# Performance work log

Hardware: AMD Instinct MI355X
Metric: run time of the kernel (lower is better)

## Reference

```python
import jax, jax.numpy as jnp
from jax import lax
import numpy as np

D_MODEL = 1024
D_STATE = 16
D_CONV = 4
EXPAND = 2
D_INNER = EXPAND * D_MODEL  # 2048
DT_RANK = D_MODEL // 16     # 64
BATCH = 4
SEQ = 1024


def setup_inputs() -> dict:
    key = jax.random.key(0)
    ks = iter(jax.random.split(key, 40))
    def w(shape, s=0.02):
        return (s * jax.random.normal(next(ks), shape)).astype(jnp.float32)
    inp = {"x": jax.random.normal(next(ks), (BATCH, SEQ, D_MODEL), dtype=jnp.float32)}
    # S4D-real style A init: A = -exp(A_log), A_log = log(1..N) per channel
    Alog = jnp.log(jnp.tile(jnp.arange(1, D_STATE + 1, dtype=jnp.float32), (D_INNER, 1)))
    for s in ("f", "b"):
        inp[f"inproj_{s}"] = w((D_MODEL, 2 * D_INNER))
        inp[f"conv_w_{s}"] = w((D_INNER, D_CONV), 0.2)
        inp[f"conv_b_{s}"] = jnp.zeros((D_INNER,), jnp.float32)
        inp[f"xproj_{s}"] = w((D_INNER, DT_RANK + 2 * D_STATE))
        inp[f"dt_w_{s}"] = w((DT_RANK, D_INNER))
        inp[f"dt_b_{s}"] = jnp.full((D_INNER,), -4.0, jnp.float32)  # softplus(-4)~0.018
        inp[f"Alog_{s}"] = Alog
        inp[f"Dp_{s}"] = jnp.ones((D_INNER,), jnp.float32)
        inp[f"outproj_{s}"] = w((D_INNER, D_MODEL))
    inp["gate_w"] = w((2 * D_MODEL, D_MODEL))
    inp["gate_b"] = jnp.zeros((D_MODEL,), jnp.float32)
    inp["proj_w"] = w((D_MODEL, D_MODEL))
    inp["proj_b"] = jnp.zeros((D_MODEL,), jnp.float32)
    return inp


def _mamba(x, inproj, conv_w, conv_b, xproj, dt_w, dt_b, Alog, Dp, outproj):
    B, L, _ = x.shape
    xz = x @ inproj                           # [B,L,2*Di]
    u, z = jnp.split(xz, 2, axis=-1)          # each [B,L,Di]
    # depthwise causal conv1d, width D_CONV
    K = conv_w.shape[1]
    up = jnp.pad(u, ((0, 0), (K - 1, 0), (0, 0)))
    uc = conv_b
    for k in range(K):
        uc = uc + up[:, k:k + L, :] * conv_w[:, k]
    uc = jax.nn.silu(uc)                      # [B,L,Di]
    dbl = uc @ xproj                          # [B,L,dt_rank+2N]
    N = Alog.shape[1]
    dt, Bm, Cm = jnp.split(dbl, [DT_RANK, DT_RANK + N], axis=-1)
    delta = jax.nn.softplus(dt @ dt_w + dt_b) # [B,L,Di]
    A = -jnp.exp(Alog)                        # [Di,N]

    def step(h, inp):
        u_t, d_t, B_t, C_t = inp              # [B,Di],[B,Di],[B,N],[B,N]
        dA = jnp.exp(d_t[..., None] * A)      # [B,Di,N]
        h = dA * h + (d_t * u_t)[..., None] * B_t[:, None, :]
        y_t = jnp.einsum('bdn,bn->bd', h, C_t)
        return h, y_t

    h0 = jnp.zeros((B, uc.shape[-1], N), x.dtype)
    xs = (uc.transpose(1, 0, 2), delta.transpose(1, 0, 2),
          Bm.transpose(1, 0, 2), Cm.transpose(1, 0, 2))
    _, ys = lax.scan(step, h0, xs)            # ys: [L,B,Di]
    y = ys.transpose(1, 0, 2) + uc * Dp
    y = y * jax.nn.silu(z)
    return y @ outproj                        # [B,L,d_model]


def reference(x, inproj_f, conv_w_f, conv_b_f, xproj_f, dt_w_f, dt_b_f, Alog_f, Dp_f, outproj_f,
              inproj_b, conv_w_b, conv_b_b, xproj_b, dt_w_b, dt_b_b, Alog_b, Dp_b, outproj_b,
              gate_w, gate_b, proj_w, proj_b):
    y_f = _mamba(x, inproj_f, conv_w_f, conv_b_f, xproj_f, dt_w_f, dt_b_f, Alog_f, Dp_f, outproj_f)
    xb = jnp.flip(x, axis=1)
    y_b = _mamba(xb, inproj_b, conv_w_b, conv_b_b, xproj_b, dt_w_b, dt_b_b, Alog_b, Dp_b, outproj_b)
    y_b = jnp.flip(y_b, axis=1)
    g = jax.nn.sigmoid(jnp.concatenate([y_f, y_b], axis=-1) @ gate_w + gate_b)
    y = g * y_f + (1.0 - g) * y_b
    return y @ proj_w + proj_b
```

## Files before the change

kernel.cpp:

```cpp
#include <hip/hip_runtime.h>
#include <hip/hip_bf16.h>

#define B_  4
#define L_  1024
#define DM  1024
#define DI  2048
#define NS  16
#define RK  64
#define MT  (B_ * L_)
#define NC  32
#define CH  (L_ / NC)
#define KSX 256
#define NZX 8
#define PSZ (B_ * NC * NS * DI)

typedef unsigned short u16;
typedef __attribute__((ext_vector_type(8))) short  bh8;
typedef __attribute__((ext_vector_type(8))) unsigned short us8;
typedef __attribute__((ext_vector_type(8))) _Float16 h8;
typedef __attribute__((ext_vector_type(4))) float  f4;

__device__ __forceinline__ float bf2f(u16 u) {
  union { unsigned int i; float f; } c; c.i = ((unsigned int)u) << 16; return c.f;
}
__device__ __forceinline__ u16 f2bf(float f) {
  union { float f; unsigned int i; } c; c.f = f;
  unsigned int x = c.i;
  unsigned int r = (x + 0x7fffu + ((x >> 16) & 1u)) >> 16;
  return (u16)r;
}

__device__ __forceinline__ void gl16(const u16* g, u16* l) {
  __builtin_amdgcn_global_load_lds(
      (const __attribute__((address_space(1))) void*)g,
      (__attribute__((address_space(3))) void*)l, 16, 0, 0);
}

__global__ void detect_k(const unsigned int* __restrict__ alog,
                         int* __restrict__ flag, int* __restrict__ afl) {
  *flag = (alog[0] != 0u) ? 1 : 0;
  afl[0] = 1; afl[1] = 1;
}

__global__ __launch_bounds__(256)
void cvt_k(const void* __restrict__ src, u16* __restrict__ dst, int n,
           const int* __restrict__ flag) {
  int i = blockIdx.x * 256 + threadIdx.x;
  if (i >= n) return;
  if (*flag) dst[i] = ((const u16*)src)[i];
  else       dst[i] = f2bf(((const float*)src)[i]);
}

__global__ __launch_bounds__(256)
void cvt10_k(const int* __restrict__ flagp,
             const void* s0, u16* d0, int n0, const void* s1, u16* d1, int n1,
             const void* s2, u16* d2, int n2, const void* s3, u16* d3, int n3,
             const void* s4, u16* d4, int n4, const void* s5, u16* d5, int n5,
             const void* s6, u16* d6, int n6, const void* s7, u16* d7, int n7,
             const void* s8, u16* d8, int n8, const void* s9, u16* d9, int n9)
{
  const void* s; u16* d; int n;
  switch (blockIdx.y) {
    case 0: s = s0; d = d0; n = n0; break;  case 1: s = s1; d = d1; n = n1; break;
    case 2: s = s2; d = d2; n = n2; break;  case 3: s = s3; d = d3; n = n3; break;
    case 4: s = s4; d = d4; n = n4; break;  case 5: s = s5; d = d5; n = n5; break;
    case 6: s = s6; d = d6; n = n6; break;  case 7: s = s7; d = d7; n = n7; break;
    case 8: s = s8; d = d8; n = n8; break;  default: s = s9; d = d9; n = n9; break;
  }
  int i = blockIdx.x * 256 + threadIdx.x;
  if (i >= n) return;
  d[i] = *flagp ? ((const u16*)s)[i] : f2bf(((const float*)s)[i]);
}

__global__ __launch_bounds__(256)
void a2_k(const int* __restrict__ flagp, const void* __restrict__ sf,
          const void* __restrict__ sb, _Float16* __restrict__ A2h,
          int* __restrict__ afl)
{
  int i = blockIdx.x * 256 + threadIdx.x;
  int dir = i >> 15;
  const void* src = dir ? sb : sf;
  int j = i & (DI * NS - 1);
  float v = *flagp ? bf2f(((const u16*)src)[j]) : ((const float*)src)[j];
  float a2 = -__expf(v);
  A2h[i] = (_Float16)a2;
  int n = i & 15;
  if (fabsf(a2 + (float)(n + 1)) > 1e-3f * (n + 1)) atomicAnd(&afl[dir], 0);
}

struct TpBatch {
  const void* src[8];
  u16* dst[8];
  int R[8], C[8], tilesX[8];
  int tOff[9];
  int cnt;
};

__global__ __launch_bounds__(256)
void tposeB_k(TpBatch tb, const int* __restrict__ flag) {
  __shared__ u16 tile[32][33];
  int bid = blockIdx.x;
  int i = 0;
  #pragma unroll
  for (int q = 0; q < 7; ++q) if (i + 1 < tb.cnt && bid >= tb.tOff[i + 1]) ++i;
  int local = bid - tb.tOff[i];
  int tX = tb.tilesX[i];
  int c0 = (local % tX) * 32, r0 = (local / tX) * 32;
  int R = tb.R[i], C = tb.C[i];
  const void* src = tb.src[i];
  u16* dst = tb.dst[i];
  int tx = threadIdx.x & 31, ty = threadIdx.x >> 5;
  int isbf = *flag;
  #pragma unroll
  for (int k = 0; k < 4; ++k) {
    int r = r0 + ty + k * 8, c = c0 + tx;
    u16 v = 0;
    if (r < R && c < C)
      v = isbf ? ((const u16*)src)[(size_t)r * C + c]
               : f2bf(((const float*)src)[(size_t)r * C + c]);
    tile[ty + k * 8][tx] = v;
  }
  __syncthreads();
  #pragma unroll
  for (int k = 0; k < 4; ++k) {
    int c = c0 + ty + k * 8, r = r0 + tx;
    if (c < C && r < R)
      dst[(size_t)c * R + r] = tile[tx][ty + k * 8];
  }
}

template<int ACT, int CATM, int OUTF, int BIDIR, int SPLITK, int DUO, int XSW, int ZDIR>
__global__ __launch_bounds__(256)
void gemm2(const u16* __restrict__ A, int lda,
           const u16* __restrict__ Wt,
           const u16* __restrict__ bias,
           void* __restrict__ Cp, int ldc, void* __restrict__ C2,
           int M, int N, int K,
           const u16* __restrict__ yfp, const u16* __restrict__ ybp,
           const int* __restrict__ flagp, const u16* __restrict__ Aalt)
{
  __shared__ __align__(16) u16 As[128][64];
  __shared__ __align__(16) u16 Bs[128][64];

  int bx, by;
  if (XSW) {
    int g = blockIdx.y * gridDim.x + blockIdx.x;
    int xcd = g & 7, j = g >> 3;
    int bxb = gridDim.x >> 3;
    int sh = 31 - __builtin_clz(bxb);
    bx = xcd * bxb + (j & (bxb - 1));
    by = j >> sh;
  } else { bx = blockIdx.x; by = blockIdx.y; }

  int zdir = 0, zslice = 0;
  if (ZDIR && SPLITK) { zdir = blockIdx.z >> 3; zslice = blockIdx.z & (NZX - 1); }
  else if (ZDIR)      { zdir = blockIdx.z; }
  else if (SPLITK)    { zslice = blockIdx.z; }

  const int tid  = threadIdx.x;
  const int lane = tid & 63;
  const int w    = tid >> 6;
  const int wm   = (w >> 1) * 64, wn = (w & 1) * 64;
  const int bm0  = by * 128, bn0 = bx * 128;
  const int l15  = lane & 15, quad = lane >> 4;
  const int rI8  = lane >> 3;
  const int cG8  = (lane & 7) ^ rI8;

  const u16* Wtp = ZDIR ? (Wt + (size_t)zdir * N * K) : Wt;

  f4 acc[4][4] = {};

  const int kb = SPLITK ? zslice * KSX : 0;
  const int ke = SPLITK ? kb + KSX : K;

  for (int k0 = kb; k0 < ke; k0 += 64) {
    {
      const u16* Abase;
      if (ZDIR)     Abase = zdir ? Aalt : A;
      else if (DUO) Abase = (bn0 < DM) ? A : ybp;
      else          Abase = A;
      #pragma unroll
      for (int t = 0; t < 4; ++t) {
        int rb = w * 32 + t * 8;
        int row = rb + rI8;
        const u16* gp;
        if (CATM) {
          int kk = k0 + cG8 * 8;
          int m = bm0 + row;
          gp = (kk < DM) ? (yfp + (size_t)m * DM + kk)
                         : (ybp + (size_t)(m ^ (L_ - 1)) * DM + (kk - DM));
        } else {
          gp = Abase + (size_t)(bm0 + row) * lda + k0 + cG8 * 8;
        }
        gl16(gp, &As[rb][0]);
      }
    }
    #pragma unroll
    for (int t = 0; t < 4; ++t) {
      int rb = w * 32 + t * 8;
      int row = rb + rI8;
      int n = bn0 + row; if (n > N - 1) n = N - 1;
      gl16(Wtp + (size_t)n * K + k0 + cG8 * 8, &Bs[rb][0]);
    }
    __syncthreads();
    #pragma unroll
    for (int s = 0; s < 2; ++s) {
      bh8 af[4], bg[4];
      const int phys = ((quad + 4 * s) ^ (l15 & 7)) * 8;
      #pragma unroll
      for (int i = 0; i < 4; ++i) {
        af[i] = *(const bh8*)&As[wm + i * 16 + l15][phys];
        bg[i] = *(const bh8*)&Bs[wn + i * 16 + l15][phys];
      }
      #pragma unroll
      for (int i = 0; i < 4; ++i)
        #pragma unroll
        for (int j = 0; j < 4; ++j)
          acc[i][j] = __builtin_amdgcn_mfma_f32_16x16x32_bf16(af[i], bg[j], acc[i][j], 0, 0, 0);
    }
    __syncthreads();
  }

  const int obf = (OUTF == 1) ? *flagp : 1;
  const size_t zoff = 0;
  #pragma unroll
  for (int j = 0; j < 4; ++j) {
    int lcol = bn0 + wn + j * 16 + l15;
    if (lcol >= N) continue;
    int col = BIDIR ? (lcol & 4095) : (DUO ? (lcol & (DM - 1)) : lcol);
    float bv = bias ? bf2f(bias[(ZDIR ? zdir * N : 0) + col]) : 0.f;
    #pragma unroll
    for (int i = 0; i < 4; ++i) {
      #pragma unroll
      for (int r = 0; r < 4; ++r) {
        int row = bm0 + wm + i * 16 + quad * 4 + r;
        float v = acc[i][j][r] + bv;
        if (ACT == 1) v = (v > 20.f) ? v : __logf(1.f + __expf(v));
        if (ACT == 3) {
          float g = 1.f / (1.f + __expf(-v));
          float fv = bf2f(yfp[(size_t)row * DM + col]);
          float bb = bf2f(ybp[(size_t)(row ^ (L_ - 1)) * DM + col]);
          v = g * fv + (1.f - g) * bb;
        }
        if (BIDIR) {
          u16* base = (lcol < 4096) ? (u16*)Cp : (u16*)C2;
          int orow = (lcol < 4096) ? row : (row ^ (L_ - 1));
          u16* dst = (col < DI) ? (base + (size_t)orow * DI + col)
                                : (base + (size_t)(8u << 20) + (size_t)orow * DI + (col - DI));
          *dst = f2bf(v);
        } else if (DUO) {
          if (lcol < DM) ((u16*)Cp)[(size_t)row * ldc + col] = f2bf(v);
          else           ((u16*)C2)[(size_t)row * ldc + col] = f2bf(v);
        } else if (ZDIR) {
          u16* base = zdir ? (u16*)C2 : (u16*)Cp;
          base[(size_t)row * ldc + col] = f2bf(v);
        } else if (OUTF == 1 && !obf) {
          ((float*)Cp)[(size_t)row * ldc + col] = v;
        } else {
          ((u16*)Cp)[(size_t)row * ldc + col] = f2bf(v);
        }
      }
    }
  }
}


__global__ __launch_bounds__(256)
void gemmxp(const u16* __restrict__ uc,
            const u16* __restrict__ Wt,
            float* __restrict__ xpf, float* __restrict__ xpb)
{
  const int by  = blockIdx.x;
  const int dir = blockIdx.y >> 3, zsl = blockIdx.y & 7;
  const int bm0 = by * 128;
  const int kb  = zsl * KSX;
  const int tid = threadIdx.x, lane = tid & 63, w = tid >> 6;
  const int wm  = (w >> 1) * 64, wn = (w & 1) * 64;
  const int l15 = lane & 15, quad = lane >> 4;
  const u16* Ab = uc + (size_t)dir * MT * DI;
  const u16* Bb = Wt + (size_t)dir * 96 * DI;

  f4 acc[4][4] = {};
  #pragma unroll
  for (int ks = 0; ks < KSX / 32; ++ks) {
    const int ko = kb + ks * 32 + quad * 8;
    bh8 a[4], b[4];
    #pragma unroll
    for (int i = 0; i < 4; ++i)
      a[i] = *(const bh8*)&Ab[(size_t)(bm0 + wm + i * 16 + l15) * DI + ko];
    #pragma unroll
    for (int j = 0; j < 4; ++j) {
      int n = wn + j * 16 + l15; if (n > 95) n = 95;
      b[j] = *(const bh8*)&Bb[(size_t)n * DI + ko];
    }
    #pragma unroll
    for (int i = 0; i < 4; ++i)
      #pragma unroll
      for (int j = 0; j < 4; ++j)
        acc[i][j] = __builtin_amdgcn_mfma_f32_16x16x32_bf16(a[i], b[j], acc[i][j], 0, 0, 0);
  }
  float* P = (dir ? xpb : xpf) + (size_t)zsl * MT * 96;
  #pragma unroll
  for (int j = 0; j < 4; ++j) {
    int col = wn + j * 16 + l15;
    if (col >= 96) continue;
    #pragma unroll
    for (int i = 0; i < 4; ++i)
      #pragma unroll
      for (int r = 0; r < 4; ++r) {
        int row = bm0 + wm + i * 16 + quad * 4 + r;
        P[(size_t)row * 96 + col] = acc[i][j][r];
      }
  }
}

__global__ __launch_bounds__(256)
void gemmdtw(const u16* __restrict__ dbl,
             const u16* __restrict__ Wt,
             const u16* __restrict__ bias,
             u16* __restrict__ Df, u16* __restrict__ Db)
{
  const int dir = blockIdx.z;
  const int bn0 = blockIdx.x * 128;
  const int bm0 = blockIdx.y * 128;
  const int tid = threadIdx.x, lane = tid & 63, w = tid >> 6;
  const int wm  = (w >> 1) * 64, wn = (w & 1) * 64;
  const int l15 = lane & 15, quad = lane >> 4;
  const u16* Ab = dbl + (size_t)dir * MT * 96;
  const u16* Bb = Wt + (size_t)dir * DI * RK;

  f4 acc[4][4] = {};
  #pragma unroll
  for (int s = 0; s < 2; ++s) {
    const int ko = s * 32 + quad * 8;
    bh8 a[4], b[4];
    #pragma unroll
    for (int i = 0; i < 4; ++i)
      a[i] = *(const bh8*)&Ab[(size_t)(bm0 + wm + i * 16 + l15) * 96 + ko];
    #pragma unroll
    for (int j = 0; j < 4; ++j)
      b[j] = *(const bh8*)&Bb[(size_t)(bn0 + wn + j * 16 + l15) * RK + ko];
    #pragma unroll
    for (int i = 0; i < 4; ++i)
      #pragma unroll
      for (int j = 0; j < 4; ++j)
        acc[i][j] = __builtin_amdgcn_mfma_f32_16x16x32_bf16(a[i], b[j], acc[i][j], 0, 0, 0);
  }
  u16* D = dir ? Db : Df;
  #pragma unroll
  for (int j = 0; j < 4; ++j) {
    int col = bn0 + wn + j * 16 + l15;
    float bv = bf2f(bias[dir * DI + col]);
    #pragma unroll
    for (int i = 0; i < 4; ++i)
      #pragma unroll
      for (int r = 0; r < 4; ++r) {
        int row = bm0 + wm + i * 16 + quad * 4 + r;
        float v = acc[i][j][r] + bv;
        v = (v > 20.f) ? v : __logf(1.f + __expf(v));
        D[(size_t)row * DI + col] = f2bf(v);
      }
  }
}

__global__ __launch_bounds__(512)
void gemm256i(const u16* __restrict__ A, int lda,
              const u16* __restrict__ Wt, int ldw,
              u16* __restrict__ Cp, u16* __restrict__ C2, int K)
{
  __shared__ __align__(16) u16 As[2][256][64];
  __shared__ __align__(16) u16 Bs[2][256][64];

  int g  = blockIdx.y * gridDim.x + blockIdx.x;
  int id = (g & 7) * ((gridDim.x * gridDim.y) >> 3) + (g >> 3);
  int bx = id >> 4;
  int by = id & 15;

  const int tid  = threadIdx.x;
  const int lane = tid & 63;
  const int w    = tid >> 6;
  const int wm2  = w >> 2;
  const int wn4  = w & 3;
  const int l15  = lane & 15, quad = lane >> 4;
  const int rI8  = lane >> 3;
  const int cG8  = (lane & 7) ^ rI8;
  const int bm0  = by * 256, bn0 = bx * 256;
  const int NT   = K >> 6;

  const u16* Ag = A  + (size_t)(bm0 + w * 8 + rI8) * lda + cG8 * 8;
  const u16* Bg = Wt + (size_t)(bn0 + w * 8 + rI8) * ldw + cG8 * 8;

  auto stA = [&](int kt, int bb, int c) {
    gl16(Ag + kt * 64 + (size_t)(c * 64) * lda, &As[bb][c * 64 + w * 8][0]);
  };
  auto stB = [&](int kt, int bb, int c) {
    gl16(Bg + kt * 64 + (size_t)(c * 64) * ldw, &Bs[bb][c * 64 + w * 8][0]);
  };

  f4 acc[8][4] = {};

  stB(0, 0, 0); stB(0, 0, 1); stB(0, 0, 2); stB(0, 0, 3);
  stA(0, 0, 0); stA(0, 0, 2); stA(0, 0, 1); stA(0, 0, 3);
  asm volatile("s_waitcnt vmcnt(2)" ::: "memory");
  __builtin_amdgcn_sched_barrier(0);
  __builtin_amdgcn_s_barrier();

  const int ph0 = ((quad    ) ^ (l15 & 7)) * 8;
  const int ph1 = ((quad + 4) ^ (l15 & 7)) * 8;

  for (int t = 0; t < NT; ++t) {
    const int p = t & 1, q = p ^ 1;
    const bool pre = (t + 1 < NT);
    bh8 af[4][2], bg[4][2], a2[4][2];

    #pragma unroll
    for (int x = 0; x < 4; ++x) {
      af[x][0] = *(const bh8*)&As[p][wm2 * 128 + x * 16 + l15][ph0];
      af[x][1] = *(const bh8*)&As[p][wm2 * 128 + x * 16 + l15][ph1];
    }
    #pragma unroll
    for (int x = 0; x < 2; ++x) {
      bg[x][0] = *(const bh8*)&Bs[p][wn4 * 64 + x * 16 + l15][ph0];
      bg[x][1] = *(const bh8*)&Bs[p][wn4 * 64 + x * 16 + l15][ph1];
    }
    if (pre) { stB(t + 1, q, 0); stB(t + 1, q, 1); }
    asm volatile("s_waitcnt lgkmcnt(8)" ::: "memory");
    __builtin_amdgcn_sched_barrier(0);
    __builtin_amdgcn_s_barrier();
    asm volatile("s_waitcnt lgkmcnt(0)" ::: "memory");
    __builtin_amdgcn_sched_barrier(0);
    __builtin_amdgcn_s_setprio(1);
    #pragma unroll
    for (int s = 0; s < 2; ++s)
      #pragma unroll
      for (int i = 0; i < 4; ++i)
        #pragma unroll
        for (int j = 0; j < 2; ++j)
          acc[i][j] = __builtin_amdgcn_mfma_f32_16x16x32_bf16(af[i][s], bg[j][s], acc[i][j], 0, 0, 0);
    __builtin_amdgcn_s_setprio(0);
    __builtin_amdgcn_sched_barrier(0);
    __builtin_amdgcn_s_barrier();

    #pragma unroll
    for (int x = 2; x < 4; ++x) {
      bg[x][0] = *(const bh8*)&Bs[p][wn4 * 64 + x * 16 + l15][ph0];
      bg[x][1] = *(const bh8*)&Bs[p][wn4 * 64 + x * 16 + l15][ph1];
    }
    if (pre) { stB(t + 1, q, 2); stB(t + 1, q, 3); }
    __builtin_amdgcn_sched_barrier(0);
    __builtin_amdgcn_s_barrier();
    asm volatile("s_waitcnt lgkmcnt(0)" ::: "memory");
    __builtin_amdgcn_sched_barrier(0);
    __builtin_amdgcn_s_setprio(1);
    #pragma unroll
    for (int s = 0; s < 2; ++s)
      #pragma unroll
      for (int i = 0; i < 4; ++i)
        #pragma unroll
        for (int j = 0; j < 2; ++j)
          acc[i][2 + j] = __builtin_amdgcn_mfma_f32_16x16x32_bf16(af[i][s], bg[2 + j][s], acc[i][2 + j], 0, 0, 0);
    __builtin_amdgcn_s_setprio(0);
    if (pre) { asm volatile("s_waitcnt vmcnt(4)" ::: "memory"); }
    else     { asm volatile("s_waitcnt vmcnt(0)" ::: "memory"); }
    __builtin_amdgcn_sched_barrier(0);
    __builtin_amdgcn_s_barrier();

    #pragma unroll
    for (int x = 0; x < 4; ++x) {
      a2[x][0] = *(const bh8*)&As[p][wm2 * 128 + 64 + x * 16 + l15][ph0];
      a2[x][1] = *(const bh8*)&As[p][wm2 * 128 + 64 + x * 16 + l15][ph1];
    }
    if (pre) { stA(t + 1, q, 0); stA(t + 1, q, 2); }
    __builtin_amdgcn_sched_barrier(0);
    __builtin_amdgcn_s_barrier();
    asm volatile("s_waitcnt lgkmcnt(0)" ::: "memory");
    __builtin_amdgcn_sched_barrier(0);
    __builtin_amdgcn_s_setprio(1);
    #pragma unroll
    for (int s = 0; s < 2; ++s)
      #pragma unroll
      for (int i = 0; i < 4; ++i)
        #pragma unroll
        for (int j = 0; j < 2; ++j)
          acc[4 + i][j] = __builtin_amdgcn_mfma_f32_16x16x32_bf16(a2[i][s], bg[j][s], acc[4 + i][j], 0, 0, 0);
    __builtin_amdgcn_s_setprio(0);
    __builtin_amdgcn_sched_barrier(0);
    __builtin_amdgcn_s_barrier();

    if (pre) { stA(t + 1, q, 1); stA(t + 1, q, 3); }
    __builtin_amdgcn_sched_barrier(0);
    __builtin_amdgcn_s_setprio(1);
    #pragma unroll
    for (int s = 0; s < 2; ++s)
      #pragma unroll
      for (int i = 0; i < 4; ++i)
        #pragma unroll
        for (int j = 0; j < 2; ++j)
          acc[4 + i][2 + j] = __builtin_amdgcn_mfma_f32_16x16x32_bf16(a2[i][s], bg[2 + j][s], acc[4 + i][2 + j], 0, 0, 0);
    __builtin_amdgcn_s_setprio(0);
    if (pre) { asm volatile("s_waitcnt vmcnt(2)" ::: "memory"); }
    else     { asm volatile("s_waitcnt vmcnt(0)" ::: "memory"); }
    __builtin_amdgcn_sched_barrier(0);
    __builtin_amdgcn_s_barrier();
  }

  {
    const int lc0  = bn0 + wn4 * 64;
    const int col0 = lc0 & 4095;
    u16* base = (lc0 < 4096) ? Cp : C2;
    u16* dst0 = (col0 < DI) ? base : (base + (size_t)(8u << 20) - DI);
    const int flip = (lc0 < 4096) ? 0 : (L_ - 1);
    #pragma unroll
    for (int i = 0; i < 8; ++i) {
      #pragma unroll
      for (int r = 0; r < 4; ++r) {
        int row = bm0 + wm2 * 128 + i * 16 + quad * 4 + r;
        u16* rp = dst0 + (size_t)(row ^ flip) * DI + col0;
        #pragma unroll
        for (int j = 0; j < 4; ++j)
          rp[j * 16 + l15] = f2bf(acc[i][j][r]);
      }
    }
  }
}

__global__ __launch_bounds__(256)
void rdbl_k(const float* __restrict__ xpf, const float* __restrict__ xpb,
            u16* __restrict__ dbl)
{
  int i = blockIdx.x * 256 + threadIdx.x;
  int dir = i >= MT * 96;
  int il = dir ? (i - MT * 96) : i;
  const float* P = dir ? xpb : xpf;
  float s = 0.f;
  #pragma unroll
  for (int z = 0; z < NZX; ++z) s += P[(size_t)z * MT * 96 + il];
  dbl[i] = f2bf(s);
}

__global__ __launch_bounds__(256)
void conv8_k(const u16* __restrict__ xzu_f, const u16* __restrict__ xzu_b,
             const u16* __restrict__ cw,
             const u16* __restrict__ cb,
             u16* __restrict__ uc)
{
  int g = blockIdx.x * 256 + threadIdx.x;
  int dir = g >> 18;
  int gl = g & ((1 << 18) - 1);
  int d  = (gl & (DI / 8 - 1)) * 8;
  int t0 = ((gl >> 8) & (L_ / 4 - 1)) * 4;
  int b  = gl >> 16;
  const u16* xzu = dir ? xzu_b : xzu_f;
  const u16* cwp = cw + dir * DI * 4;
  const u16* cbp = cb + dir * DI;
  float w[8][4], bias[8];
  {
    u16 wr[32];
    #pragma unroll
    for (int q = 0; q < 4; ++q)
      *(us8*)&wr[q * 8] = *(const us8*)&cwp[d * 4 + q * 8];
    #pragma unroll
    for (int i = 0; i < 8; ++i)
      #pragma unroll
      for (int k = 0; k < 4; ++k) w[i][k] = bf2f(wr[i * 4 + k]);
    us8 cbv = *(const us8*)&cbp[d];
    #pragma unroll
    for (int i = 0; i < 8; ++i) bias[i] = bf2f(cbv[i]);
  }
  float xv[7][8];
  #pragma unroll
  for (int r = 0; r < 7; ++r) {
    int ts = t0 + r - 3;
    if (ts >= 0) {
      us8 v = *(const us8*)&xzu[(size_t)(b * L_ + ts) * DI + d];
      #pragma unroll
      for (int i = 0; i < 8; ++i) xv[r][i] = bf2f(v[i]);
    } else {
      #pragma unroll
      for (int i = 0; i < 8; ++i) xv[r][i] = 0.f;
    }
  }
  #pragma unroll
  for (int o = 0; o < 4; ++o) {
    us8 out;
    #pragma unroll
    for (int i = 0; i < 8; ++i) {
      float a = bias[i];
      #pragma unroll
      for (int k = 0; k < 4; ++k) a += xv[o + k][i] * w[i][k];
      out[i] = f2bf(a / (1.f + __expf(-a)));
    }
    *(us8*)&uc[(size_t)dir * MT * DI + (size_t)(b * L_ + t0 + o) * DI + d] = out;
  }
}

__global__ __launch_bounds__(256, 4)
void scanA_k(const u16* __restrict__ delta, const u16* __restrict__ uc,
             const u16* __restrict__ dbl, const _Float16* __restrict__ A2h,
             const int* __restrict__ afl,
             _Float16* __restrict__ P, _Float16* __restrict__ S)
{
  int g = blockIdx.x * 256 + threadIdx.x;
  int dir = g >> 18;
  int gl = g & ((1 << 18) - 1);
  int d = gl & (DI - 1);
  int c = (gl >> 11) & (NC - 1);
  int b = gl >> 16;
  delta += (size_t)dir * MT * DI;
  uc    += (size_t)dir * MT * DI;
  dbl   += (size_t)dir * MT * 96;
  P     += (size_t)dir * PSZ;
  S     += (size_t)dir * PSZ;
  const int fast = afl[dir];
  float A2[NS];
  if (!fast) {
    h8 a0 = *(const h8*)&A2h[((size_t)dir * DI + d) * NS];
    h8 a1 = *(const h8*)&A2h[((size_t)dir * DI + d) * NS + 8];
    #pragma unroll
    for (int n = 0; n < 8; ++n) { A2[n] = (float)a0[n]; A2[n + 8] = (float)a1[n]; }
  }
  float Pv[NS], Sv[NS];
  #pragma unroll
  for (int n = 0; n < NS; ++n) { Pv[n] = 1.f; Sv[n] = 0.f; }
  int t0 = c * CH;
  for (int t = t0; t < t0 + CH; ++t) {
    size_t row = (size_t)b * L_ + t;
    float dv = bf2f(delta[row * DI + d]);
    float uv = bf2f(uc[row * DI + d]);
    float du = dv * uv;
    us8 b0 = *(const us8*)&dbl[row * 96 + 64];
    us8 b1 = *(const us8*)&dbl[row * 96 + 72];
    if (fast) {
      float q = __expf(-dv);
      float dA = 1.f;
      #pragma unroll
      for (int n = 0; n < NS; ++n) {
        dA *= q;
        float Bv = (n < 8) ? bf2f(b0[n & 7]) : bf2f(b1[n & 7]);
        Sv[n] = fmaf(dA, Sv[n], du * Bv);
        Pv[n] *= dA;
      }
    } else {
      #pragma unroll
      for (int n = 0; n < NS; ++n) {
        float Bv = (n < 8) ? bf2f(b0[n & 7]) : bf2f(b1[n & 7]);
        float dA = __expf(dv * A2[n]);
        Sv[n] = fmaf(dA, Sv[n], du * Bv);
        Pv[n] *= dA;
      }
    }
  }
  size_t base = ((size_t)(b * NC + c) * NS) * DI + d;
  #pragma unroll
  for (int n = 0; n < NS; ++n) {
    P[base + (size_t)n * DI] = (_Float16)Pv[n];
    S[base + (size_t)n * DI] = (_Float16)Sv[n];
  }
}

__global__ __launch_bounds__(256)
void scanB_k(_Float16* __restrict__ P, const _Float16* __restrict__ S)
{
  int g = blockIdx.x * 256 + threadIdx.x;
  int dir = g >> 17;
  int gl = g & ((1 << 17) - 1);
  int d = gl & (DI - 1);
  int n = (gl >> 11) & (NS - 1);
  int b = gl >> 15;
  P += (size_t)dir * PSZ;
  S += (size_t)dir * PSZ;
  float h = 0.f;
  #pragma unroll 4
  for (int c = 0; c < NC; ++c) {
    size_t ix = ((size_t)(b * NC + c) * NS + n) * DI + d;
    float p = (float)P[ix], s = (float)S[ix];
    P[ix] = (_Float16)h;
    h = fmaf(p, h, s);
  }
}

__global__ __launch_bounds__(256, 4)
void scanC_k(const u16* __restrict__ uc, const u16* delta,
             const u16* __restrict__ dbl, const u16* __restrict__ xzz_f,
             const u16* __restrict__ xzz_b, const _Float16* __restrict__ A2h,
             const int* __restrict__ afl, const u16* __restrict__ Dp,
             const _Float16* __restrict__ hstart, u16* ys)
{
  int g = blockIdx.x * 256 + threadIdx.x;
  int dir = g >> 18;
  int gl = g & ((1 << 18) - 1);
  int d = gl & (DI - 1);
  int c = (gl >> 11) & (NC - 1);
  int b = gl >> 16;
  const u16* xzz = dir ? xzz_b : xzz_f;
  uc     += (size_t)dir * MT * DI;
  delta  += (size_t)dir * MT * DI;
  dbl    += (size_t)dir * MT * 96;
  Dp     += dir * DI;
  hstart += (size_t)dir * PSZ;
  ys     += (size_t)dir * MT * DI;
  const int fast = afl[dir];
  float A2[NS], h[NS];
  if (!fast) {
    h8 a0 = *(const h8*)&A2h[((size_t)dir * DI + d) * NS];
    h8 a1 = *(const h8*)&A2h[((size_t)dir * DI + d) * NS + 8];
    #pragma unroll
    for (int n = 0; n < 8; ++n) { A2[n] = (float)a0[n]; A2[n + 8] = (float)a1[n]; }
  }
  float Dv = bf2f(Dp[d]);
  size_t hbase = ((size_t)(b * NC + c) * NS) * DI + d;
  #pragma unroll
  for (int n = 0; n < NS; ++n) h[n] = (float)hstart[hbase + (size_t)n * DI];
  int t0 = c * CH;
  for (int t = t0; t < t0 + CH; ++t) {
    size_t row = (size_t)b * L_ + t;
    float dv = bf2f(delta[row * DI + d]);
    float uv = bf2f(uc[row * DI + d]);
    float du = dv * uv;
    us8 b0 = *(const us8*)&dbl[row * 96 + 64];
    us8 b1 = *(const us8*)&dbl[row * 96 + 72];
    us8 c0 = *(const us8*)&dbl[row * 96 + 80];
    us8 c1 = *(const us8*)&dbl[row * 96 + 88];
    float y = 0.f;
    if (fast) {
      float q = __expf(-dv);
      float dA = 1.f;
      #pragma unroll
      for (int n = 0; n < NS; ++n) {
        dA *= q;
        float Bv = (n < 8) ? bf2f(b0[n & 7]) : bf2f(b1[n & 7]);
        float Cv = (n < 8) ? bf2f(c0[n & 7]) : bf2f(c1[n & 7]);
        h[n] = fmaf(dA, h[n], du * Bv);
        y = fmaf(h[n], Cv, y);
      }
    } else {
      #pragma unroll
      for (int n = 0; n < NS; ++n) {
        float Bv = (n < 8) ? bf2f(b0[n & 7]) : bf2f(b1[n & 7]);
        float Cv = (n < 8) ? bf2f(c0[n & 7]) : bf2f(c1[n & 7]);
        float dA = __expf(dv * A2[n]);
        h[n] = fmaf(dA, h[n], du * Bv);
        y = fmaf(h[n], Cv, y);
      }
    }
    float z = bf2f(xzz[row * DI + d]);
    float out = (y + uv * Dv) * (z / (1.f + __expf(-z)));
    ys[row * DI + d] = f2bf(out);
  }
}

extern "C" void kernel_launch(void* const* d_in, const int* in_sizes, int n_in,
                              void* d_out, int out_size, void* d_ws, size_t ws_size,
                              hipStream_t stream)
{
  char* ws = (char*)d_ws;
  const size_t MB = 1ull << 20;
  const size_t KB = 1024;

  u16* xzu_f   = (u16*)(ws + 0);
  u16* xzz_f   = (u16*)(ws + 16 * MB);
  u16* xzu_b   = (u16*)(ws + 32 * MB);
  u16* xzz_b   = (u16*)(ws + 48 * MB);
  u16* uc      = (u16*)(ws + 64 * MB);
  u16* delta_f = (u16*)(ws + 96 * MB);
  u16* delta_b = (u16*)(ws + 112 * MB);
  u16* dbl     = (u16*)(ws + 128 * MB);
  char* SM     = ws + 128 * MB + 1536 * KB;
  u16* w_convw = (u16*)(SM);
  u16* w_convb = (u16*)(SM + 32 * KB);
  u16* w_dtb   = (u16*)(SM + 40 * KB);
  u16* w_dp    = (u16*)(SM + 48 * KB);
  u16* w_gb    = (u16*)(SM + 56 * KB);
  u16* w_pb    = (u16*)(SM + 58 * KB);
  int* flag    = (int*)(SM + 60 * KB);
  int* afl     = (int*)(SM + 60 * KB + 8);
  _Float16* A2h = (_Float16*)(ws + 128 * MB + 1600 * KB);
  u16* xproj_t2 = (u16*)(ws + 128 * MB + 1728 * KB);
  u16* dtw_t2   = (u16*)(ws + 128 * MB + 2496 * KB);
  u16* xc       = uc;
  u16* inproj_t = delta_f;
  float* xpart_f = (float*)delta_f;
  float* xpart_b = (float*)delta_b;
  _Float16* Pb   = (_Float16*)xzu_f;
  _Float16* Sb   = (_Float16*)xzu_b;
  u16* outp2_t  = (u16*)(ws + 80 * MB);
  u16* gw_t     = (u16*)(ws + 88 * MB);
  u16* pw_t     = (u16*)(ws + 92 * MB);
  u16* yf       = xzz_f;
  u16* yb       = xzz_b;
  u16* yc       = (u16*)(ws + 0);

  dim3 blk(256);
  detect_k<<<1, 1, 0, stream>>>((const unsigned int*)d_in[7], flag, afl);

  cvt10_k<<<dim3(32, 10), blk, 0, stream>>>(flag,
      d_in[2],  w_convw,            DI * 4, d_in[3],  w_convb,      DI,
      d_in[6],  w_dtb,              DI,     d_in[8],  w_dp,         DI,
      d_in[11], w_convw + DI * 4,   DI * 4, d_in[12], w_convb + DI, DI,
      d_in[15], w_dtb + DI,         DI,     d_in[17], w_dp + DI,    DI,
      d_in[20], w_gb,               DM,     d_in[22], w_pb,         DM);
  a2_k<<<2 * DI * NS / 256, blk, 0, stream>>>(flag, d_in[7], d_in[16], A2h, afl);
  cvt_k<<<MT * DM / 256, blk, 0, stream>>>(d_in[0], xc, MT * DM, flag);

  {
    TpBatch tb{};
    auto add = [&](int i, const void* s, u16* d, int R, int C) {
      tb.src[i] = s; tb.dst[i] = d; tb.R[i] = R; tb.C[i] = C;
      tb.tilesX[i] = (C + 31) / 32;
      tb.tOff[i + 1] = tb.tOff[i] + tb.tilesX[i] * ((R + 31) / 32);
    };
    tb.tOff[0] = 0;
    add(0, d_in[1],  inproj_t,               DM, 2 * DI);
    add(1, d_in[10], inproj_t + 4096 * 1024, DM, 2 * DI);
    add(2, d_in[4],  xproj_t2,               DI, 96);
    add(3, d_in[13], xproj_t2 + 96 * 2048,   DI, 96);
    add(4, d_in[5],  dtw_t2,                 RK, DI);
    add(5, d_in[14], dtw_t2 + 2048 * 64,     RK, DI);
    tb.cnt = 6;
    tposeB_k<<<tb.tOff[6], blk, 0, stream>>>(tb, flag);
  }

  gemm256i<<<dim3(32, 16), dim3(512), 0, stream>>>(
      xc, DM, inproj_t, DM, xzu_f, xzu_b, DM);

  conv8_k<<<2 * MT * DI / 32 / 256, blk, 0, stream>>>(
      xzu_f, xzu_b, w_convw, w_convb, uc);

  gemmxp<<<dim3(32, 2 * NZX), blk, 0, stream>>>(uc, xproj_t2, xpart_f, xpart_b);
  rdbl_k<<<2 * MT * 96 / 256, blk, 0, stream>>>(xpart_f, xpart_b, dbl);

  gemmdtw<<<dim3(16, 32, 2), blk, 0, stream>>>(dbl, dtw_t2, w_dtb,
                                               delta_f, delta_b);

  scanA_k<<<2 * B_ * NC * DI / 256, blk, 0, stream>>>(
      delta_f, uc, dbl, A2h, afl, Pb, Sb);
  scanB_k<<<2 * B_ * NS * DI / 256, blk, 0, stream>>>(Pb, Sb);
  scanC_k<<<2 * B_ * NC * DI / 256, blk, 0, stream>>>(
      uc, delta_f, dbl, xzz_f, xzz_b, A2h, afl, w_dp, Pb, delta_f);

  {
    TpBatch tb{};
    auto add = [&](int i, const void* s, u16* d, int R, int C) {
      tb.src[i] = s; tb.dst[i] = d; tb.R[i] = R; tb.C[i] = C;
      tb.tilesX[i] = (C + 31) / 32;
      tb.tOff[i + 1] = tb.tOff[i] + tb.tilesX[i] * ((R + 31) / 32);
    };
    tb.tOff[0] = 0;
    add(0, d_in[9],  outp2_t,               DI, DM);
    add(1, d_in[18], outp2_t + 1024 * 2048, DI, DM);
    add(2, d_in[19], gw_t,                  2 * DM, DM);
    add(3, d_in[21], pw_t,                  DM, DM);
    tb.cnt = 4;
    tposeB_k<<<tb.tOff[4], blk, 0, stream>>>(tb, flag);
  }

  gemm2<0, 0, 0, 0, 0, 1, 1, 0><<<dim3(16, 32), blk, 0, stream>>>(
      delta_f, DI, outp2_t, nullptr, yf, DM, yb, MT, 2 * DM, DI,
      nullptr, delta_b, flag, nullptr);

  gemm2<3, 1, 0, 0, 0, 0, 1, 0><<<dim3(8, 32), blk, 0, stream>>>(
      yf, DM, gw_t, w_gb, yc, DM, nullptr, MT, DM, 2 * DM, yf, yb, flag, nullptr);
  gemm2<0, 0, 1, 0, 0, 0, 1, 0><<<dim3(8, 32), blk, 0, stream>>>(
      yc, DM, pw_t, w_pb, d_out, DM, nullptr, MT, DM, DM,
      nullptr, nullptr, flag, nullptr);
}
```

Before: 561.8 us.

## Restructure bidirectional GEMM main loop with single barrier and register prefetch

Replaces the four-phase, four-barrier GEMM inner loop with a simpler schedule. All A/B tiles for the next K-step are issued at once, MFMAs are grouped by K-half, and there is one __syncthreads per iteration. The first fragments for the next step are loaded into registers right after that barrier. The aim is to cut barrier and waitcnt overhead and overlap LDS reads with MFMA. The trade-off is less careful interleaving of global loads with compute, since the full barrier now waits on all outstanding loads mid-iteration, and higher register pressure.

Result: faster. 550.6 us (-2.0%).

```diff
diff --git a/kernel.cpp b/kernel.cpp
--- a/kernel.cpp
+++ b/kernel.cpp
@@ -222,7 +222,6 @@
   }
 
   const int obf = (OUTF == 1) ? *flagp : 1;
-  const size_t zoff = 0;
   #pragma unroll
   for (int j = 0; j < 4; ++j) {
     int lcol = bn0 + wn + j * 16 + l15;
@@ -390,118 +389,88 @@
   const u16* Ag = A  + (size_t)(bm0 + w * 8 + rI8) * lda + cG8 * 8;
   const u16* Bg = Wt + (size_t)(bn0 + w * 8 + rI8) * ldw + cG8 * 8;
 
-  auto stA = [&](int kt, int bb, int c) {
-    gl16(Ag + kt * 64 + (size_t)(c * 64) * lda, &As[bb][c * 64 + w * 8][0]);
+  auto STAGE = [&](int kt, int bb) {
+    const u16* ap = Ag + kt * 64;
+    const u16* bp = Bg + kt * 64;
+    #pragma unroll
+    for (int i = 0; i < 4; ++i) {
+      gl16(ap + (size_t)(i * 64) * lda, &As[bb][i * 64 + w * 8][0]);
+      gl16(bp + (size_t)(i * 64) * ldw, &Bs[bb][i * 64 + w * 8][0]);
+    }
   };
-  auto stB = [&](int kt, int bb, int c) {
-    gl16(Bg + kt * 64 + (size_t)(c * 64) * ldw, &Bs[bb][c * 64 + w * 8][0]);
-  };
 
   f4 acc[8][4] = {};
-
-  stB(0, 0, 0); stB(0, 0, 1); stB(0, 0, 2); stB(0, 0, 3);
-  stA(0, 0, 0); stA(0, 0, 2); stA(0, 0, 1); stA(0, 0, 3);
-  asm volatile("s_waitcnt vmcnt(2)" ::: "memory");
-  __builtin_amdgcn_sched_barrier(0);
-  __builtin_amdgcn_s_barrier();
 
   const int ph0 = ((quad    ) ^ (l15 & 7)) * 8;
   const int ph1 = ((quad + 4) ^ (l15 & 7)) * 8;
 
+  STAGE(0, 0);
+  __syncthreads();
+
+  bh8 aA[4], aB[4], aC[4], aD[4], bg0[4], bg1[4];
+  #pragma unroll
+  for (int x = 0; x < 4; ++x) {
+    aA[x]  = *(const bh8*)&As[0][wm2 * 128 + x * 16 + l15][ph0];
+    bg0[x] = *(const bh8*)&Bs[0][wn4 * 64  + x * 16 + l15][ph0];
+  }
+
+  #pragma unroll 2
   for (int t = 0; t < NT; ++t) {
     const int p = t & 1, q = p ^ 1;
     const bool pre = (t + 1 < NT);
-    bh8 af[4][2], bg[4][2], a2[4][2];
+
+    if (pre) STAGE(t + 1, q);
+
+    #pragma unroll
+    for (int x = 0; x < 4; ++x)
+      aB[x] = *(const bh8*)&As[p][wm2 * 128 + 64 + x * 16 + l15][ph0];
+    __builtin_amdgcn_s_setprio(1);
+    #pragma unroll
+    for (int i = 0; i < 4; ++i)
+      #pragma unroll
+      for (int j = 0; j < 4; ++j)
+        acc[i][j] = __builtin_amdgcn_mfma_f32_16x16x32_bf16(aA[i], bg0[j], acc[i][j], 0, 0, 0);
+    __builtin_amdgcn_s_setprio(0);
 
     #pragma unroll
     for (int x = 0; x < 4; ++x) {
-      af[x][0] = *(const bh8*)&As[p][wm2 * 128 + x * 16 + l15][ph0];
-      af[x][1] = *(const bh8*)&As[p][wm2 * 128 + x * 16 + l15][ph1];
-    }
-    #pragma unroll
-    for (int x = 0; x < 2; ++x) {
-      bg[x][0] = *(const bh8*)&Bs[p][wn4 * 64 + x * 16 + l15][ph0];
-      bg[x][1] = *(const bh8*)&Bs[p][wn4 * 64 + x * 16 + l15][ph1];
-    }
-    if (pre) { stB(t + 1, q, 0); stB(t + 1, q, 1); }
-    asm volatile("s_waitcnt lgkmcnt(8)" ::: "memory");
-    __builtin_amdgcn_sched_barrier(0);
-    __builtin_amdgcn_s_barrier();
-    asm volatile("s_waitcnt lgkmcnt(0)" ::: "memory");
-    __builtin_amdgcn_sched_barrier(0);
+      aC[x]  = *(const bh8*)&As[p][wm2 * 128 + x * 16 + l15][ph1];
+      bg1[x] = *(const bh8*)&Bs[p][wn4 * 64  + x * 16 + l15][ph1];
+    }
     __builtin_amdgcn_s_setprio(1);
     #pragma unroll
-    for (int s = 0; s < 2; ++s)
-      #pragma unroll
-      for (int i = 0; i < 4; ++i)
-        #pragma unroll
-        for (int j = 0; j < 2; ++j)
-          acc[i][j] = __builtin_amdgcn_mfma_f32_16x16x32_bf16(af[i][s], bg[j][s], acc[i][j], 0, 0, 0);
+    for (int i = 0; i < 4; ++i)
+      #pragma unroll
+      for (int j = 0; j < 4; ++j)
+        acc[4 + i][j] = __builtin_amdgcn_mfma_f32_16x16x32_bf16(aB[i], bg0[j], acc[4 + i][j], 0, 0, 0);
     __builtin_amdgcn_s_setprio(0);
-    __builtin_amdgcn_sched_barrier(0);
-    __builtin_amdgcn_s_barrier();
-
-    #pragma unroll
-    for (int x = 2; x < 4; ++x) {
-      bg[x][0] = *(const bh8*)&Bs[p][wn4 * 64 + x * 16 + l15][ph0];
-      bg[x][1] = *(const bh8*)&Bs[p][wn4 * 64 + x * 16 + l15][ph1];
-    }
-    if (pre) { stB(t + 1, q, 2); stB(t + 1, q, 3); }
-    __builtin_amdgcn_sched_barrier(0);
-    __builtin_amdgcn_s_barrier();
-    asm volatile("s_waitcnt lgkmcnt(0)" ::: "memory");
-    __builtin_amdgcn_sched_barrier(0);
+
+    #pragma unroll
+    for (int x = 0; x < 4; ++x)
+      aD[x] = *(const bh8*)&As[p][wm2 * 128 + 64 + x * 16 + l15][ph1];
     __builtin_amdgcn_s_setprio(1);
     #pragma unroll
-    for (int s = 0; s < 2; ++s)
-      #pragma unroll
-      for (int i = 0; i < 4; ++i)
-        #pragma unroll
-        for (int j = 0; j < 2; ++j)
-          acc[i][2 + j] = __builtin_amdgcn_mfma_f32_16x16x32_bf16(af[i][s], bg[2 + j][s], acc[i][2 + j], 0, 0, 0);
+    for (int i = 0; i < 4; ++i)
+      #pragma unroll
+      for (int j = 0; j < 4; ++j)
+        acc[i][j] = __builtin_amdgcn_mfma_f32_16x16x32_bf16(aC[i], bg1[j], acc[i][j], 0, 0, 0);
     __builtin_amdgcn_s_setprio(0);
-    if (pre) { asm volatile("s_waitcnt vmcnt(4)" ::: "memory"); }
-    else     { asm volatile("s_waitcnt vmcnt(0)" ::: "memory"); }
-    __builtin_amdgcn_sched_barrier(0);
-    __builtin_amdgcn_s_barrier();
-
-    #pragma unroll
-    for (int x = 0; x < 4; ++x) {
-      a2[x][0] = *(const bh8*)&As[p][wm2 * 128 + 64 + x * 16 + l15][ph0];
-      a2[x][1] = *(const bh8*)&As[p][wm2 * 128 + 64 + x * 16 + l15][ph1];
-    }
-    if (pre) { stA(t + 1, q, 0); stA(t + 1, q, 2); }
-    __builtin_amdgcn_sched_barrier(0);
-    __builtin_amdgcn_s_barrier();
-    asm volatile("s_waitcnt lgkmcnt(0)" ::: "memory");
-    __builtin_amdgcn_sched_barrier(0);
+
+    __syncthreads();
+    if (pre) {
+      #pragma unroll
+      for (int x = 0; x < 4; ++x) {
+        aA[x]  = *(const bh8*)&As[q][wm2 * 128 + x * 16 + l15][ph0];
+        bg0[x] = *(const bh8*)&Bs[q][wn4 * 64  + x * 16 + l15][ph0];
+      }
+    }
     __builtin_amdgcn_s_setprio(1);
     #pragma unroll
-    for (int s = 0; s < 2; ++s)
-      #pragma unroll
-      for (int i = 0; i < 4; ++i)
-        #pragma unroll
-        for (int j = 0; j < 2; ++j)
-          acc[4 + i][j] = __builtin_amdgcn_mfma_f32_16x16x32_bf16(a2[i][s], bg[j][s], acc[4 + i][j], 0, 0, 0);
+    for (int i = 0; i < 4; ++i)
+      #pragma unroll
+      for (int j = 0; j < 4; ++j)
+        acc[4 + i][j] = __builtin_amdgcn_mfma_f32_16x16x32_bf16(aD[i], bg1[j], acc[4 + i][j], 0, 0, 0);
     __builtin_amdgcn_s_setprio(0);
-    __builtin_amdgcn_sched_barrier(0);
-    __builtin_amdgcn_s_barrier();
-
-    if (pre) { stA(t + 1, q, 1); stA(t + 1, q, 3); }
-    __builtin_amdgcn_sched_barrier(0);
-    __builtin_amdgcn_s_setprio(1);
-    #pragma unroll
-    for (int s = 0; s < 2; ++s)
-      #pragma unroll
-      for (int i = 0; i < 4; ++i)
-        #pragma unroll
-        for (int j = 0; j < 2; ++j)
-          acc[4 + i][2 + j] = __builtin_amdgcn_mfma_f32_16x16x32_bf16(a2[i][s], bg[2 + j][s], acc[4 + i][2 + j], 0, 0, 0);
-    __builtin_amdgcn_s_setprio(0);
-    if (pre) { asm volatile("s_waitcnt vmcnt(2)" ::: "memory"); }
-    else     { asm volatile("s_waitcnt vmcnt(0)" ::: "memory"); }
-    __builtin_amdgcn_sched_barrier(0);
-    __builtin_amdgcn_s_barrier();
   }
 
   {
```
